# Optimization experiments

Hardware: AMD Instinct MI355X
Metric: run time of the kernel (lower is better)

Reference implementation:

```python
import jax, jax.numpy as jnp
import numpy as np

B, T, F, OUT = 32, 8192, 128, 1024

def setup_inputs() -> dict:
    key = jax.random.key(0)
    kx, kl = jax.random.split(key)
    x = jax.random.normal(kx, (B, T, F), dtype=jnp.float32)
    # true (unpadded) lengths; module assumes max(lengths) == T (padded length)
    lengths = jax.random.randint(kl, (B,), OUT + 1, T + 1)
    lengths = lengths.at[0].set(T)
    return {"x": x, "lengths": lengths, "output_size": OUT}

def reference(x, lengths, output_size):
    # Original math: per-sample box filter of length f_b = lengths_b - output_size + 1
    # (ones / f_b, zero-padded to max) applied as grouped conv over time:
    #   out[b, t, f] = (1/f_b) * sum_{k=0}^{f_b-1} x[b, t+k, f],  t in [0, output_size)
    # Implemented via prefix sums instead of materializing the sparse filter bank.
    fsize = lengths - output_size + 1                                  # [B]
    cs = jnp.cumsum(x, axis=1)                                         # [B, T, F]
    cs = jnp.concatenate([jnp.zeros_like(cs[:, :1]), cs], axis=1)      # [B, T+1, F]
    t = jnp.arange(output_size)                                        # [OUT]
    idx = (t[None, :] + fsize[:, None])[:, :, None]                    # [B, OUT, 1]
    hi = jnp.take_along_axis(cs, idx, axis=1)                          # [B, OUT, F]
    lo = cs[:, :output_size, :]                                        # [B, OUT, F]
    return (hi - lo) / fsize[:, None, None].astype(x.dtype)
```

## Files before the change

kernel.cpp:

```cpp
#include <hip/hip_runtime.h>

#define NB    32
#define NT    8192
#define NF    128
#define NOUT  1024
#define SEGSZ 32
#define NSEG  256
#define TILE  32
#define NTILE (NOUT/TILE)

__device__ __forceinline__ float4 f4add(float4 a, float4 b) {
  return make_float4(a.x + b.x, a.y + b.y, a.z + b.z, a.w + b.w);
}
__device__ __forceinline__ float4 f4sub(float4 a, float4 b) {
  return make_float4(a.x - b.x, a.y - b.y, a.z - b.z, a.w - b.w);
}

__global__ __launch_bounds__(256) void seg_sums(const float* __restrict__ x,
                                                const int* __restrict__ lengths,
                                                float* __restrict__ S) {
  const int bid  = blockIdx.x;
  const int task = (bid >> 3) | ((bid & 7) << 9);
  const int b    = task >> 7;
  const int h    = task & 127;
  const int len  = lengths[b];
  if (h * 64 >= len) return;

  const int tid = threadIdx.x;
  const int fl  = tid & 31;
  const int tl  = tid >> 5;

  const float4* xp =
      reinterpret_cast<const float4*>(x + (size_t)b * NT * NF +
                                      (size_t)(h * 64) * NF) + fl;
  float4 acc = make_float4(0.f, 0.f, 0.f, 0.f);
  #pragma unroll
  for (int r = 0; r < 8; ++r)
    acc = f4add(acc, xp[(tl * 8 + r) * 32]);

  __shared__ float4 red[8][32];
  red[tl][fl] = acc;
  __syncthreads();
  if (tl == 0) {
    float4 s = f4add(f4add(red[0][fl], red[1][fl]),
                     f4add(red[2][fl], red[3][fl]));
    reinterpret_cast<float4*>(S + ((size_t)b * NSEG + h * 2) * NF)[fl] = s;
  } else if (tl == 4) {
    float4 s = f4add(f4add(red[4][fl], red[5][fl]),
                     f4add(red[6][fl], red[7][fl]));
    reinterpret_cast<float4*>(S + ((size_t)b * NSEG + h * 2 + 1) * NF)[fl] = s;
  }
}

__global__ __launch_bounds__(256) void window_avg(const float* __restrict__ x,
                                                  const int* __restrict__ lengths,
                                                  const float* __restrict__ S,
                                                  float* __restrict__ out) {
  const int wg   = ((blockIdx.x & 7) << 7) + (blockIdx.x >> 3);
  const int b    = wg >> 5;
  const int tile = wg & (NTILE - 1);
  const int len  = lengths[b];
  const int W    = len - NOUT + 1;
  const int t0   = tile * TILE;
  const int p1   = t0 + W;
  const int s_hi = p1 >> 5;

  const int tid = threadIdx.x;
  const int fl  = tid & 31;
  const int tl  = tid >> 5;

  const float4* xb =
      reinterpret_cast<const float4*>(x + (size_t)b * NT * NF) + fl;
  const float4* Sb =
      reinterpret_cast<const float4*>(S + (size_t)b * NSEG * NF) + fl;

  float4 acc = make_float4(0.f, 0.f, 0.f, 0.f);
  for (int s = tile + tl; s < s_hi; s += 8)
    acc = f4add(acc, Sb[s * 32]);
  for (int j = (s_hi << 5) + tl; j < p1; j += 8)
    acc = f4add(acc, xb[j * 32]);

  __shared__ float4 red[8][32];
  red[tl][fl] = acc;
  __syncthreads();
  float4 A = make_float4(0.f, 0.f, 0.f, 0.f);
  #pragma unroll
  for (int k = 0; k < 8; ++k) A = f4add(A, red[k][fl]);
  __syncthreads();

  float4 D = make_float4(0.f, 0.f, 0.f, 0.f);
  if (tl < 7) {
    const int baseLo = t0 + 4 * tl;
    const int baseHi = p1 + 4 * tl;
    #pragma unroll
    for (int j = 0; j < 4; ++j) {
      float4 h = xb[(baseHi + j) * 32];
      float4 l = xb[(baseLo + j) * 32];
      D = f4add(D, f4sub(h, l));
    }
  }
  red[tl][fl] = D;
  __syncthreads();
  #pragma unroll
  for (int k = 0; k < 7; ++k)
    if (k < tl) A = f4add(A, red[k][fl]);

  const float invW  = 1.0f / (float)W;
  const int   tbase = t0 + 4 * tl;
  float4* ob =
      reinterpret_cast<float4*>(out + ((size_t)b * NOUT + tbase) * NF) + fl;

  #pragma unroll
  for (int i = 0; i < 4; ++i) {
    ob[i * 32] = make_float4(A.x * invW, A.y * invW, A.z * invW, A.w * invW);
    if (i < 3) {
      float4 h = xb[(tbase + i + W) * 32];
      float4 l = xb[(tbase + i) * 32];
      A = f4add(A, f4sub(h, l));
    }
  }
}

extern "C" void kernel_launch(void* const* d_in, const int* in_sizes, int n_in,
                              void* d_out, int out_size, void* d_ws, size_t ws_size,
                              hipStream_t stream) {
  const float* x       = (const float*)d_in[0];
  const int*   lengths = (const int*)d_in[1];
  float*       S       = (float*)d_ws;
  float*       out     = (float*)d_out;

  hipLaunchKernelGGL(seg_sums, dim3(NB * 128), dim3(256), 0, stream,
                     x, lengths, S);
  hipLaunchKernelGGL(window_avg, dim3(NB * NTILE), dim3(256), 0, stream,
                     x, lengths, S, out);
}
```

Baseline: 33.59 us.

## Add 128-row group sums to shorten window prefix accumulation loop

```diff
diff --git a/kernel.cpp b/kernel.cpp
--- a/kernel.cpp
+++ b/kernel.cpp
@@ -4,8 +4,8 @@
 #define NT    8192
 #define NF    128
 #define NOUT  1024
-#define SEGSZ 32
 #define NSEG  256
+#define NGRP  64
 #define TILE  32
 #define NTILE (NOUT/TILE)
 
@@ -18,13 +18,13 @@
 
 __global__ __launch_bounds__(256) void seg_sums(const float* __restrict__ x,
                                                 const int* __restrict__ lengths,
-                                                float* __restrict__ S) {
-  const int bid  = blockIdx.x;
-  const int task = (bid >> 3) | ((bid & 7) << 9);
-  const int b    = task >> 7;
-  const int h    = task & 127;
-  const int len  = lengths[b];
-  if (h * 64 >= len) return;
+                                                float* __restrict__ S32,
+                                                float* __restrict__ S128) {
+  const int blk = blockIdx.x;
+  const int b   = blk >> 6;
+  const int g   = blk & 63;
+  const int len = lengths[b];
+  if (g * 128 >= len) return;
 
   const int tid = threadIdx.x;
   const int fl  = tid & 31;
@@ -32,29 +32,31 @@
 
   const float4* xp =
       reinterpret_cast<const float4*>(x + (size_t)b * NT * NF +
-                                      (size_t)(h * 64) * NF) + fl;
+                                      (size_t)(g * 128) * NF) + fl;
   float4 acc = make_float4(0.f, 0.f, 0.f, 0.f);
   #pragma unroll
-  for (int r = 0; r < 8; ++r)
-    acc = f4add(acc, xp[(tl * 8 + r) * 32]);
+  for (int r = 0; r < 16; ++r)
+    acc = f4add(acc, xp[(tl * 16 + r) * 32]);
 
   __shared__ float4 red[8][32];
   red[tl][fl] = acc;
   __syncthreads();
-  if (tl == 0) {
+  if (tl < 4) {
+    float4 s = f4add(red[2 * tl][fl], red[2 * tl + 1][fl]);
+    reinterpret_cast<float4*>(S32 + ((size_t)b * NSEG + g * 4 + tl) * NF)[fl] = s;
+  } else if (tl == 4) {
     float4 s = f4add(f4add(red[0][fl], red[1][fl]),
                      f4add(red[2][fl], red[3][fl]));
-    reinterpret_cast<float4*>(S + ((size_t)b * NSEG + h * 2) * NF)[fl] = s;
-  } else if (tl == 4) {
-    float4 s = f4add(f4add(red[4][fl], red[5][fl]),
-                     f4add(red[6][fl], red[7][fl]));
-    reinterpret_cast<float4*>(S + ((size_t)b * NSEG + h * 2 + 1) * NF)[fl] = s;
+    s = f4add(s, f4add(f4add(red[4][fl], red[5][fl]),
+                       f4add(red[6][fl], red[7][fl])));
+    reinterpret_cast<float4*>(S128 + ((size_t)b * NGRP + g) * NF)[fl] = s;
   }
 }
 
 __global__ __launch_bounds__(256) void window_avg(const float* __restrict__ x,
                                                   const int* __restrict__ lengths,
-                                                  const float* __restrict__ S,
+                                                  const float* __restrict__ S32,
+                                                  const float* __restrict__ S128,
                                                   float* __restrict__ out) {
   const int wg   = ((blockIdx.x & 7) << 7) + (blockIdx.x >> 3);
   const int b    = wg >> 5;
@@ -64,6 +66,8 @@
   const int t0   = tile * TILE;
   const int p1   = t0 + W;
   const int s_hi = p1 >> 5;
+  const int g_lo = (t0 + 127) >> 7;
+  const int g_hi = p1 >> 7;
 
   const int tid = threadIdx.x;
   const int fl  = tid & 31;
@@ -71,12 +75,23 @@
 
   const float4* xb =
       reinterpret_cast<const float4*>(x + (size_t)b * NT * NF) + fl;
-  const float4* Sb =
-      reinterpret_cast<const float4*>(S + (size_t)b * NSEG * NF) + fl;
+  const float4* S32b =
+      reinterpret_cast<const float4*>(S32 + (size_t)b * NSEG * NF) + fl;
+  const float4* S128b =
+      reinterpret_cast<const float4*>(S128 + (size_t)b * NGRP * NF) + fl;
 
   float4 acc = make_float4(0.f, 0.f, 0.f, 0.f);
-  for (int s = tile + tl; s < s_hi; s += 8)
-    acc = f4add(acc, Sb[s * 32]);
+  if (g_hi > g_lo) {
+    for (int s = tile + tl; s < 4 * g_lo; s += 8)
+      acc = f4add(acc, S32b[s * 32]);
+    for (int g = g_lo + tl; g < g_hi; g += 8)
+      acc = f4add(acc, S128b[g * 32]);
+    for (int s = 4 * g_hi + tl; s < s_hi; s += 8)
+      acc = f4add(acc, S32b[s * 32]);
+  } else {
+    for (int s = tile + tl; s < s_hi; s += 8)
+      acc = f4add(acc, S32b[s * 32]);
+  }
   for (int j = (s_hi << 5) + tl; j < p1; j += 8)
     acc = f4add(acc, xb[j * 32]);
 
@@ -126,11 +141,12 @@
                               hipStream_t stream) {
   const float* x       = (const float*)d_in[0];
   const int*   lengths = (const int*)d_in[1];
-  float*       S       = (float*)d_ws;
+  float*       S32     = (float*)d_ws;
+  float*       S128    = (float*)d_ws + (size_t)NB * NSEG * NF;
   float*       out     = (float*)d_out;
 
-  hipLaunchKernelGGL(seg_sums, dim3(NB * 128), dim3(256), 0, stream,
-                     x, lengths, S);
+  hipLaunchKernelGGL(seg_sums, dim3(NB * NGRP), dim3(256), 0, stream,
+                     x, lengths, S32, S128);
   hipLaunchKernelGGL(window_avg, dim3(NB * NTILE), dim3(256), 0, stream,
-                     x, lengths, S, out);
+                     x, lengths, S32, S128, out);
 }
```

Measured after the change: 29.46 us. -12.3%, faster.
